# Optimization experiments

Measured on AMD Instinct MI355X. Metric: run time of the kernel, lower is better.

The kernel has to match this reference:

```python
import jax, jax.numpy as jnp
import numpy as np

N_NODES = 50000
N_EDGES = 800000
C_IN = 128
C_OUT = 64
C_HID = 2 * C_OUT  # 128


def setup_inputs() -> dict:
    key = jax.random.key(0)
    ks = jax.random.split(key, 8)
    x = jax.random.normal(ks[0], (N_NODES, C_IN), dtype=jnp.float32)
    edge_index = jax.random.randint(ks[1], (2, N_EDGES), 0, N_NODES, dtype=jnp.int64)
    s1 = 1.0 / np.sqrt(C_IN)
    s2 = 1.0 / np.sqrt(C_HID)
    s3 = 1.0 / np.sqrt(C_OUT)
    W1 = jax.random.uniform(ks[2], (C_IN, C_HID), jnp.float32, -s1, s1)
    b1 = jnp.zeros((C_HID,), jnp.float32)
    W2 = jax.random.uniform(ks[3], (C_HID, C_OUT), jnp.float32, -s2, s2)
    b2 = jnp.zeros((C_OUT,), jnp.float32)
    Wb = jax.random.uniform(ks[4], (1, C_OUT, C_OUT), jnp.float32, -s3, s3)
    bb = jax.random.uniform(ks[5], (1,), jnp.float32, -s3, s3)
    return {"x": x, "edge_index": edge_index, "W1": W1, "b1": b1,
            "W2": W2, "b2": b2, "Wb": Wb, "bb": bb}


def gcn_conv(x, W, b, src, dst, n_nodes):
    # PyG GCNConv: h = x @ W; add self-loops; symmetric normalization D^-1/2 (A+I) D^-1/2.
    h = x @ W  # [N, F]
    ones = jnp.ones((src.shape[0],), h.dtype)
    deg = jax.ops.segment_sum(ones, dst, num_segments=n_nodes) + 1.0  # +1 for self-loop
    dinv = jax.lax.rsqrt(deg)
    norm = dinv[src] * dinv[dst]  # [E]
    msgs = h[src] * norm[:, None]  # [E, F]
    agg = jax.ops.segment_sum(msgs, dst, num_segments=n_nodes)
    # self-loop contribution: norm_ii = 1/deg_i
    agg = agg + h * (1.0 / deg)[:, None]
    return agg + b


def reference(x, edge_index, W1, b1, W2, b2, Wb, bb):
    src = edge_index[0]
    dst = edge_index[1]
    n = x.shape[0]
    # encode
    h = jax.nn.relu(gcn_conv(x, W1, b1, src, dst, n))
    z = gcn_conv(h, W2, b2, src, dst, n)  # [N, C_OUT]
    # decode: bilinear on (z[src], z[dst]) -> sigmoid
    zs = z[src]  # [E, C_OUT]
    zd = z[dst]  # [E, C_OUT]
    logits = jnp.einsum('ec,ocd,ed->eo', zs, Wb, zd) + bb  # [E, 1]
    return jax.nn.sigmoid(logits)
```

## Files before the change

### kernel.cpp

```cpp
#include <hip/hip_runtime.h>
#include <hip/hip_bf16.h>


#define N_NODES 50000
#define BSH 7
#define BSZ 128
#define NBUCK ((N_NODES + BSZ - 1) / BSZ)
#define EPB 4096

typedef unsigned int u32;
typedef unsigned short u16;

typedef __attribute__((ext_vector_type(8))) short bf16x8;
typedef __attribute__((ext_vector_type(4))) float f32x4;
union frag_u { bf16x8 f; u32 u[4]; uint4 v; };

__device__ __forceinline__ float bflo(u32 u) { return __uint_as_float(u << 16); }
__device__ __forceinline__ float bfhi(u32 u) { return __uint_as_float(u & 0xffff0000u); }
__device__ __forceinline__ u32 f2bf(float f) {
    u32 b = __float_as_uint(f);
    return (b + 0x7fffu + ((b >> 16) & 1u)) >> 16;
}
__device__ __forceinline__ u32 pack2(float a, float b) { return f2bf(a) | (f2bf(b) << 16); }

__global__ __launch_bounds__(256) void bucket_hist(const int* __restrict__ dst,
                                                   int* __restrict__ bhist, int E) {
    __shared__ int hist[NBUCK];
    for (int i = threadIdx.x; i < NBUCK; i += 256) hist[i] = 0;
    __syncthreads();
    int base = blockIdx.x * EPB;
    int e1 = min(base + EPB, E);
    for (int e = base + threadIdx.x; e < e1; e += 256)
        atomicAdd(&hist[dst[e] >> BSH], 1);
    __syncthreads();
    for (int b = threadIdx.x; b < NBUCK; b += 256) {
        int c = hist[b];
        if (c) atomicAdd(&bhist[b], c);
    }
}

__global__ __launch_bounds__(512) void bucket_scan(const int* __restrict__ bhist,
                                                   int* __restrict__ bbase,
                                                   int* __restrict__ bcur, int E) {
    __shared__ int tmp[512];
    int t = threadIdx.x;
    int v = (t < NBUCK) ? bhist[t] : 0;
    tmp[t] = v;
    __syncthreads();
    for (int off = 1; off < 512; off <<= 1) {
        int a = (t >= off) ? tmp[t - off] : 0;
        __syncthreads();
        tmp[t] += a;
        __syncthreads();
    }
    int excl = tmp[t] - v;
    if (t < NBUCK) { bbase[t] = excl; bcur[t] = excl; }
    if (t == 0) bbase[NBUCK] = E;
}

__global__ __launch_bounds__(256) void bucket_scatter(const int* __restrict__ src,
                                                      const int* __restrict__ dst,
                                                      int* __restrict__ bcur,
                                                      u32* __restrict__ pair, int E) {
    __shared__ int hist[NBUCK];
    for (int i = threadIdx.x; i < NBUCK; i += 256) hist[i] = 0;
    __syncthreads();
    int base = blockIdx.x * EPB;
    int s_[16], d_[16];
#pragma unroll
    for (int it = 0; it < 16; it++) {
        int e = base + it * 256 + threadIdx.x;
        if (e < E) {
            s_[it] = src[e];
            d_[it] = dst[e];
            atomicAdd(&hist[d_[it] >> BSH], 1);
        } else {
            d_[it] = -1;
        }
    }
    __syncthreads();
    for (int b = threadIdx.x; b < NBUCK; b += 256) {
        int c = hist[b];
        hist[b] = c ? atomicAdd(&bcur[b], c) : 0;
    }
    __syncthreads();
#pragma unroll
    for (int it = 0; it < 16; it++) {
        if (d_[it] >= 0) {
            int b = d_[it] >> BSH;
            int off = atomicAdd(&hist[b], 1);
            pair[off] = (u32)s_[it] | ((u32)(d_[it] & (BSZ - 1)) << 16);
        }
    }
}

__global__ __launch_bounds__(256) void bucket_sort(const u32* __restrict__ pair,
                                                   const int* __restrict__ bbase,
                                                   int* __restrict__ row_ptr,
                                                   int* __restrict__ col,
                                                   float* __restrict__ dinv,
                                                   float* __restrict__ inv, int n, int E) {
    __shared__ int cnt[BSZ];
    __shared__ int scn[BSZ];
    __shared__ int cur[BSZ];
    int t = threadIdx.x;
    int base = blockIdx.x << BSH;
    int nn = min(BSZ, n - base);
    int b0 = bbase[blockIdx.x];
    int b1 = bbase[blockIdx.x + 1];
    if (t < BSZ) cnt[t] = 0;
    __syncthreads();
    for (int j = b0 + t; j < b1; j += 256)
        atomicAdd(&cnt[pair[j] >> 16], 1);
    __syncthreads();
    if (t < BSZ) scn[t] = cnt[t];
    __syncthreads();
    for (int off = 1; off < BSZ; off <<= 1) {
        int a = (t < BSZ && t >= off) ? scn[t - off] : 0;
        __syncthreads();
        if (t < BSZ) scn[t] += a;
        __syncthreads();
    }
    if (t < nn) {
        int excl = b0 + scn[t] - cnt[t];
        row_ptr[base + t] = excl;
        cur[t] = excl;
        float d = (float)cnt[t] + 1.0f;
        dinv[base + t] = rsqrtf(d);
        inv[base + t] = 1.0f / d;
    }
    if (t == 0 && blockIdx.x == NBUCK - 1) row_ptr[n] = E;
    __syncthreads();
    for (int j = b0 + t; j < b1; j += 256) {
        u32 p = pair[j];
        int ln = (int)(p >> 16);
        int pos = atomicAdd(&cur[ln], 1);
        col[pos] = (int)(p & 0xffffu);
    }
}

template <int K, int NOUT, bool A_BF16>
__global__ __launch_bounds__(256) void gemm_mfma(const void* __restrict__ Xv,
                                                 const float* __restrict__ W,
                                                 u16* __restrict__ O, int n_rows) {
    constexpr int KP = K + 8;
    constexpr int NT = NOUT / 16;
    constexpr int KS = K / 32;
    __shared__ __align__(16) u16 Wt_hi[NOUT * KP];
    __shared__ __align__(16) u16 Wt_lo[NOUT * KP];
    int t = threadIdx.x;
    for (int i4 = t; i4 < K * NOUT / 4; i4 += 256) {
        int k = (i4 * 4) / NOUT;
        int n0 = (i4 * 4) % NOUT;
        float4 w4 = *(const float4*)&W[(size_t)k * NOUT + n0];
        float wv[4] = {w4.x, w4.y, w4.z, w4.w};
#pragma unroll
        for (int q = 0; q < 4; q++) {
            u32 hi = f2bf(wv[q]);
            u32 lo = f2bf(wv[q] - bflo(hi));
            Wt_hi[(n0 + q) * KP + k] = (u16)hi;
            Wt_lo[(n0 + q) * KP + k] = (u16)lo;
        }
    }
    __syncthreads();

    int wave = t >> 6;
    int lane = t & 63;
    int m16 = lane & 15;
    int quad = lane >> 4;
    int row0 = blockIdx.x * 128 + wave * 32;

    f32x4 acc[2][NT] = {};
    for (int ks = 0; ks < KS; ks++) {
        frag_u a_hi[2], a_lo[2];
#pragma unroll
        for (int mt = 0; mt < 2; mt++) {
            int row = row0 + mt * 16 + m16;
            row = row < n_rows ? row : n_rows - 1;
            if (A_BF16) {
                a_hi[mt].v = *(const uint4*)((const u16*)Xv + (size_t)row * K + ks * 32 + quad * 8);
            } else {
                const float* X = (const float*)Xv + (size_t)row * K + ks * 32 + quad * 8;
                float4 x0 = *(const float4*)X;
                float4 x1 = *(const float4*)(X + 4);
                float xv[8] = {x0.x, x0.y, x0.z, x0.w, x1.x, x1.y, x1.z, x1.w};
#pragma unroll
                for (int p = 0; p < 4; p++) {
                    u32 h0 = f2bf(xv[2 * p]), h1 = f2bf(xv[2 * p + 1]);
                    a_hi[mt].u[p] = h0 | (h1 << 16);
                    a_lo[mt].u[p] = pack2(xv[2 * p] - bflo(h0), xv[2 * p + 1] - bflo(h1));
                }
            }
        }
#pragma unroll
        for (int nt = 0; nt < NT; nt++) {
            int n = nt * 16 + m16;
            frag_u b_hi, b_lo;
            b_hi.v = *(const uint4*)&Wt_hi[n * KP + ks * 32 + quad * 8];
            b_lo.v = *(const uint4*)&Wt_lo[n * KP + ks * 32 + quad * 8];
#pragma unroll
            for (int mt = 0; mt < 2; mt++) {
                acc[mt][nt] = __builtin_amdgcn_mfma_f32_16x16x32_bf16(a_hi[mt].f, b_hi.f, acc[mt][nt], 0, 0, 0);
                acc[mt][nt] = __builtin_amdgcn_mfma_f32_16x16x32_bf16(a_hi[mt].f, b_lo.f, acc[mt][nt], 0, 0, 0);
                if (!A_BF16)
                    acc[mt][nt] = __builtin_amdgcn_mfma_f32_16x16x32_bf16(a_lo[mt].f, b_hi.f, acc[mt][nt], 0, 0, 0);
            }
        }
    }
#pragma unroll
    for (int mt = 0; mt < 2; mt++)
#pragma unroll
        for (int nt = 0; nt < NT; nt++)
#pragma unroll
            for (int r = 0; r < 4; r++) {
                int row = row0 + mt * 16 + quad * 4 + r;
                if (row < n_rows)
                    O[(size_t)row * NOUT + nt * 16 + m16] = (u16)f2bf(acc[mt][nt][r]);
            }
}

template <int C, bool RELU>
__global__ __launch_bounds__(256) void agg_pull(const u16* __restrict__ H,
                                                const int* __restrict__ row_ptr,
                                                const int* __restrict__ col,
                                                const float* __restrict__ dinv,
                                                const float* __restrict__ inv,
                                                const float* __restrict__ b,
                                                u16* __restrict__ O, int n) {
    constexpr int TPN = C / 8;
    const uint4* Hv = (const uint4*)H;
    int tid = blockIdx.x * 256 + threadIdx.x;
    int node = tid / TPN;
    if (node >= n) return;
    int part = tid % TPN;
    int c8 = part * 8;
    float dn = dinv[node];
    float iv = inv[node];
    float acc[8];
    {
        uint4 h = Hv[(size_t)node * TPN + part];
        acc[0] = bflo(h.x) * iv + b[c8 + 0];
        acc[1] = bfhi(h.x) * iv + b[c8 + 1];
        acc[2] = bflo(h.y) * iv + b[c8 + 2];
        acc[3] = bfhi(h.y) * iv + b[c8 + 3];
        acc[4] = bflo(h.z) * iv + b[c8 + 4];
        acc[5] = bfhi(h.z) * iv + b[c8 + 5];
        acc[6] = bflo(h.w) * iv + b[c8 + 6];
        acc[7] = bfhi(h.w) * iv + b[c8 + 7];
    }
    int j = row_ptr[node];
    int end = row_ptr[node + 1];
    for (; j + 3 < end; j += 4) {
        int s0 = col[j], s1 = col[j + 1], s2 = col[j + 2], s3 = col[j + 3];
        float n0 = dn * dinv[s0], n1 = dn * dinv[s1];
        float n2 = dn * dinv[s2], n3 = dn * dinv[s3];
        uint4 v0 = Hv[(size_t)s0 * TPN + part];
        uint4 v1 = Hv[(size_t)s1 * TPN + part];
        uint4 v2 = Hv[(size_t)s2 * TPN + part];
        uint4 v3 = Hv[(size_t)s3 * TPN + part];
        acc[0] += bflo(v0.x) * n0 + bflo(v1.x) * n1 + bflo(v2.x) * n2 + bflo(v3.x) * n3;
        acc[1] += bfhi(v0.x) * n0 + bfhi(v1.x) * n1 + bfhi(v2.x) * n2 + bfhi(v3.x) * n3;
        acc[2] += bflo(v0.y) * n0 + bflo(v1.y) * n1 + bflo(v2.y) * n2 + bflo(v3.y) * n3;
        acc[3] += bfhi(v0.y) * n0 + bfhi(v1.y) * n1 + bfhi(v2.y) * n2 + bfhi(v3.y) * n3;
        acc[4] += bflo(v0.z) * n0 + bflo(v1.z) * n1 + bflo(v2.z) * n2 + bflo(v3.z) * n3;
        acc[5] += bfhi(v0.z) * n0 + bfhi(v1.z) * n1 + bfhi(v2.z) * n2 + bfhi(v3.z) * n3;
        acc[6] += bflo(v0.w) * n0 + bflo(v1.w) * n1 + bflo(v2.w) * n2 + bflo(v3.w) * n3;
        acc[7] += bfhi(v0.w) * n0 + bfhi(v1.w) * n1 + bfhi(v2.w) * n2 + bfhi(v3.w) * n3;
    }
    for (; j < end; j++) {
        int s = col[j];
        float nm = dn * dinv[s];
        uint4 v = Hv[(size_t)s * TPN + part];
        acc[0] += bflo(v.x) * nm; acc[1] += bfhi(v.x) * nm;
        acc[2] += bflo(v.y) * nm; acc[3] += bfhi(v.y) * nm;
        acc[4] += bflo(v.z) * nm; acc[5] += bfhi(v.z) * nm;
        acc[6] += bflo(v.w) * nm; acc[7] += bfhi(v.w) * nm;
    }
    if (RELU) {
#pragma unroll
        for (int i = 0; i < 8; i++) acc[i] = fmaxf(acc[i], 0.f);
    }
    uint4 o;
    o.x = pack2(acc[0], acc[1]);
    o.y = pack2(acc[2], acc[3]);
    o.z = pack2(acc[4], acc[5]);
    o.w = pack2(acc[6], acc[7]);
    ((uint4*)O)[(size_t)node * TPN + part] = o;
}

__global__ __launch_bounds__(256) void decode_kernel(const u16* __restrict__ Y,
                                                     const u16* __restrict__ Z,
                                                     const int* __restrict__ src,
                                                     const int* __restrict__ dst,
                                                     const float* __restrict__ bb,
                                                     float* __restrict__ out, int E) {
    const uint4* Yv = (const uint4*)Y;
    const uint4* Zv = (const uint4*)Z;
    int tid = blockIdx.x * 256 + threadIdx.x;
    int e = tid / 8;
    int lane = tid % 8;
    if (e >= E) return;
    int s = src[e], d = dst[e];
    uint4 y = Yv[(size_t)s * 8 + lane];
    uint4 z = Zv[(size_t)d * 8 + lane];
    float p = bflo(y.x) * bflo(z.x) + bfhi(y.x) * bfhi(z.x)
            + bflo(y.y) * bflo(z.y) + bfhi(y.y) * bfhi(z.y)
            + bflo(y.z) * bflo(z.z) + bfhi(y.z) * bfhi(z.z)
            + bflo(y.w) * bflo(z.w) + bfhi(y.w) * bfhi(z.w);
    p += __shfl_down(p, 4, 8);
    p += __shfl_down(p, 2, 8);
    p += __shfl_down(p, 1, 8);
    if (lane == 0) out[e] = 1.0f / (1.0f + expf(-(p + bb[0])));
}

extern "C" void kernel_launch(void* const* d_in, const int* in_sizes, int n_in,
                              void* d_out, int out_size, void* d_ws, size_t ws_size,
                              hipStream_t stream) {
    const float* x  = (const float*)d_in[0];
    const int*   ei = (const int*)d_in[1];
    const float* W1 = (const float*)d_in[2];
    const float* b1 = (const float*)d_in[3];
    const float* W2 = (const float*)d_in[4];
    const float* b2 = (const float*)d_in[5];
    const float* Wb = (const float*)d_in[6];
    const float* bb = (const float*)d_in[7];
    float* out = (float*)d_out;

    const int N = N_NODES;
    const int E = in_sizes[1] / 2;
    const int* src = ei;
    const int* dst = ei + E;
    const int GBLK = (N + 127) / 128;
    const int SBLK = (E + EPB - 1) / EPB;

    char* w = (char*)d_ws;
    int*   bhist   = (int*)w;   w += (size_t)512 * 4;
    int*   bbase   = (int*)w;   w += (size_t)512 * 4;
    int*   bcur    = (int*)w;   w += (size_t)512 * 4;
    int*   row_ptr = (int*)w;   w += (size_t)(N + 1) * 4;
    int*   col     = (int*)w;   w += (size_t)E * 4;
    u32*   pair    = (u32*)w;   w += (size_t)E * 4;
    float* dinv    = (float*)w; w += (size_t)N * 4;
    float* inv     = (float*)w; w += (size_t)N * 4;
    w = (char*)(((size_t)w + 15) & ~(size_t)15);
    u16* bufA = (u16*)w;        w += (size_t)N * 128 * 2;
    u16* bufB = (u16*)w;        w += (size_t)N * 128 * 2;
    u16* bufC = (u16*)w;

    u16* H1 = bufA;
    u16* h1 = bufB;
    u16* H2 = bufA;
    u16* Z  = bufC;
    u16* Y  = bufA + (size_t)N * 64;

    hipMemsetAsync(bhist, 0, 512 * 4, stream);
    bucket_hist<<<SBLK, 256, 0, stream>>>(dst, bhist, E);
    bucket_scan<<<1, 512, 0, stream>>>(bhist, bbase, bcur, E);
    bucket_scatter<<<SBLK, 256, 0, stream>>>(src, dst, bcur, pair, E);
    bucket_sort<<<NBUCK, 256, 0, stream>>>(pair, bbase, row_ptr, col, dinv, inv, N, E);

    gemm_mfma<128, 128, false><<<GBLK, 256, 0, stream>>>(x, W1, H1, N);
    agg_pull<128, true><<<((size_t)N * 16 + 255) / 256, 256, 0, stream>>>(
        H1, row_ptr, col, dinv, inv, b1, h1, N);

    gemm_mfma<128, 64, true><<<GBLK, 256, 0, stream>>>(h1, W2, H2, N);
    agg_pull<64, false><<<((size_t)N * 8 + 255) / 256, 256, 0, stream>>>(
        H2, row_ptr, col, dinv, inv, b2, Z, N);

    gemm_mfma<64, 64, true><<<GBLK, 256, 0, stream>>>(Z, Wb, Y, N);
    decode_kernel<<<((size_t)E * 8 + 255) / 256, 256, 0, stream>>>(Y, Z, src, dst, bb, out, E);
}
```

Baseline: 259.8 us.

## Fuse dense projections into aggregation kernels and drop bucket histogram pass

The second and third GEMMs (h1@W2 and Z@Wb) are folded into the epilogues of the two aggregation kernels. Each block stages its aggregated rows in shared memory and multiplies by the weights in fp32 FMA. This removes two MFMA launches and the global round trips of h1 and Z. Separately, the bucket histogram pass is dropped: edges are scattered into fixed-capacity per-bucket slots (CAP=3072) and the scan runs on the final counts. This risks overflow if a bucket ever gets more than CAP edges, and the fused epilogue uses scalar FMAs instead of matrix cores.

Result: slower. 292.0 us (+12.4%).

```diff
diff --git a/kernel.cpp b/kernel.cpp
--- a/kernel.cpp
+++ b/kernel.cpp
@@ -7,6 +7,7 @@
 #define BSZ 128
 #define NBUCK ((N_NODES + BSZ - 1) / BSZ)
 #define EPB 4096
+#define CAP 3072
 
 typedef unsigned int u32;
 typedef unsigned short u16;
@@ -22,41 +23,6 @@
     return (b + 0x7fffu + ((b >> 16) & 1u)) >> 16;
 }
 __device__ __forceinline__ u32 pack2(float a, float b) { return f2bf(a) | (f2bf(b) << 16); }
-
-__global__ __launch_bounds__(256) void bucket_hist(const int* __restrict__ dst,
-                                                   int* __restrict__ bhist, int E) {
-    __shared__ int hist[NBUCK];
-    for (int i = threadIdx.x; i < NBUCK; i += 256) hist[i] = 0;
-    __syncthreads();
-    int base = blockIdx.x * EPB;
-    int e1 = min(base + EPB, E);
-    for (int e = base + threadIdx.x; e < e1; e += 256)
-        atomicAdd(&hist[dst[e] >> BSH], 1);
-    __syncthreads();
-    for (int b = threadIdx.x; b < NBUCK; b += 256) {
-        int c = hist[b];
-        if (c) atomicAdd(&bhist[b], c);
-    }
-}
-
-__global__ __launch_bounds__(512) void bucket_scan(const int* __restrict__ bhist,
-                                                   int* __restrict__ bbase,
-                                                   int* __restrict__ bcur, int E) {
-    __shared__ int tmp[512];
-    int t = threadIdx.x;
-    int v = (t < NBUCK) ? bhist[t] : 0;
-    tmp[t] = v;
-    __syncthreads();
-    for (int off = 1; off < 512; off <<= 1) {
-        int a = (t >= off) ? tmp[t - off] : 0;
-        __syncthreads();
-        tmp[t] += a;
-        __syncthreads();
-    }
-    int excl = tmp[t] - v;
-    if (t < NBUCK) { bbase[t] = excl; bcur[t] = excl; }
-    if (t == 0) bbase[NBUCK] = E;
-}
 
 __global__ __launch_bounds__(256) void bucket_scatter(const int* __restrict__ src,
                                                       const int* __restrict__ dst,
@@ -81,7 +47,7 @@
     __syncthreads();
     for (int b = threadIdx.x; b < NBUCK; b += 256) {
         int c = hist[b];
-        hist[b] = c ? atomicAdd(&bcur[b], c) : 0;
+        hist[b] = c ? (b * CAP + atomicAdd(&bcur[b], c)) : 0;
     }
     __syncthreads();
 #pragma unroll
@@ -92,6 +58,23 @@
             pair[off] = (u32)s_[it] | ((u32)(d_[it] & (BSZ - 1)) << 16);
         }
     }
+}
+
+__global__ __launch_bounds__(512) void bucket_scan(const int* __restrict__ bcur,
+                                                   int* __restrict__ bbase, int E) {
+    __shared__ int tmp[512];
+    int t = threadIdx.x;
+    int v = (t < NBUCK) ? bcur[t] : 0;
+    tmp[t] = v;
+    __syncthreads();
+    for (int off = 1; off < 512; off <<= 1) {
+        int a = (t >= off) ? tmp[t - off] : 0;
+        __syncthreads();
+        tmp[t] += a;
+        __syncthreads();
+    }
+    if (t < NBUCK) bbase[t] = tmp[t] - v;
+    if (t == 0) bbase[NBUCK] = E;
 }
 
 __global__ __launch_bounds__(256) void bucket_sort(const u32* __restrict__ pair,
@@ -107,11 +90,12 @@
     int base = blockIdx.x << BSH;
     int nn = min(BSZ, n - base);
     int b0 = bbase[blockIdx.x];
-    int b1 = bbase[blockIdx.x + 1];
+    int cntE = bbase[blockIdx.x + 1] - b0;
+    int p0 = blockIdx.x * CAP;
     if (t < BSZ) cnt[t] = 0;
     __syncthreads();
-    for (int j = b0 + t; j < b1; j += 256)
-        atomicAdd(&cnt[pair[j] >> 16], 1);
+    for (int j = t; j < cntE; j += 256)
+        atomicAdd(&cnt[pair[p0 + j] >> 16], 1);
     __syncthreads();
     if (t < BSZ) scn[t] = cnt[t];
     __syncthreads();
@@ -131,16 +115,16 @@
     }
     if (t == 0 && blockIdx.x == NBUCK - 1) row_ptr[n] = E;
     __syncthreads();
-    for (int j = b0 + t; j < b1; j += 256) {
-        u32 p = pair[j];
+    for (int j = t; j < cntE; j += 256) {
+        u32 p = pair[p0 + j];
         int ln = (int)(p >> 16);
         int pos = atomicAdd(&cur[ln], 1);
         col[pos] = (int)(p & 0xffffu);
     }
 }
 
-template <int K, int NOUT, bool A_BF16>
-__global__ __launch_bounds__(256) void gemm_mfma(const void* __restrict__ Xv,
+template <int K, int NOUT>
+__global__ __launch_bounds__(256) void gemm_mfma(const float* __restrict__ X,
                                                  const float* __restrict__ W,
                                                  u16* __restrict__ O, int n_rows) {
     constexpr int KP = K + 8;
@@ -177,19 +161,15 @@
         for (int mt = 0; mt < 2; mt++) {
             int row = row0 + mt * 16 + m16;
             row = row < n_rows ? row : n_rows - 1;
-            if (A_BF16) {
-                a_hi[mt].v = *(const uint4*)((const u16*)Xv + (size_t)row * K + ks * 32 + quad * 8);
-            } else {
-                const float* X = (const float*)Xv + (size_t)row * K + ks * 32 + quad * 8;
-                float4 x0 = *(const float4*)X;
-                float4 x1 = *(const float4*)(X + 4);
-                float xv[8] = {x0.x, x0.y, x0.z, x0.w, x1.x, x1.y, x1.z, x1.w};
-#pragma unroll
-                for (int p = 0; p < 4; p++) {
-                    u32 h0 = f2bf(xv[2 * p]), h1 = f2bf(xv[2 * p + 1]);
-                    a_hi[mt].u[p] = h0 | (h1 << 16);
-                    a_lo[mt].u[p] = pack2(xv[2 * p] - bflo(h0), xv[2 * p + 1] - bflo(h1));
-                }
+            const float* Xp = X + (size_t)row * K + ks * 32 + quad * 8;
+            float4 x0 = *(const float4*)Xp;
+            float4 x1 = *(const float4*)(Xp + 4);
+            float xv[8] = {x0.x, x0.y, x0.z, x0.w, x1.x, x1.y, x1.z, x1.w};
+#pragma unroll
+            for (int p = 0; p < 4; p++) {
+                u32 h0 = f2bf(xv[2 * p]), h1 = f2bf(xv[2 * p + 1]);
+                a_hi[mt].u[p] = h0 | (h1 << 16);
+                a_lo[mt].u[p] = pack2(xv[2 * p] - bflo(h0), xv[2 * p + 1] - bflo(h1));
             }
         }
 #pragma unroll
@@ -202,8 +182,7 @@
             for (int mt = 0; mt < 2; mt++) {
                 acc[mt][nt] = __builtin_amdgcn_mfma_f32_16x16x32_bf16(a_hi[mt].f, b_hi.f, acc[mt][nt], 0, 0, 0);
                 acc[mt][nt] = __builtin_amdgcn_mfma_f32_16x16x32_bf16(a_hi[mt].f, b_lo.f, acc[mt][nt], 0, 0, 0);
-                if (!A_BF16)
-                    acc[mt][nt] = __builtin_amdgcn_mfma_f32_16x16x32_bf16(a_lo[mt].f, b_hi.f, acc[mt][nt], 0, 0, 0);
+                acc[mt][nt] = __builtin_amdgcn_mfma_f32_16x16x32_bf16(a_lo[mt].f, b_hi.f, acc[mt][nt], 0, 0, 0);
             }
         }
     }
@@ -219,73 +198,168 @@
             }
 }
 
-template <int C, bool RELU>
-__global__ __launch_bounds__(256) void agg_pull(const u16* __restrict__ H,
-                                                const int* __restrict__ row_ptr,
-                                                const int* __restrict__ col,
-                                                const float* __restrict__ dinv,
-                                                const float* __restrict__ inv,
-                                                const float* __restrict__ b,
-                                                u16* __restrict__ O, int n) {
-    constexpr int TPN = C / 8;
+__global__ __launch_bounds__(256) void agg1_fused(const u16* __restrict__ H,
+                                                  const int* __restrict__ row_ptr,
+                                                  const int* __restrict__ col,
+                                                  const float* __restrict__ dinv,
+                                                  const float* __restrict__ inv,
+                                                  const float* __restrict__ b1,
+                                                  const float* __restrict__ W2,
+                                                  u16* __restrict__ H2, int n) {
+    __shared__ float h1s[16][129];
     const uint4* Hv = (const uint4*)H;
-    int tid = blockIdx.x * 256 + threadIdx.x;
-    int node = tid / TPN;
-    if (node >= n) return;
-    int part = tid % TPN;
+    int t = threadIdx.x;
+    int nl = t / 16;
+    int part = t % 16;
     int c8 = part * 8;
-    float dn = dinv[node];
-    float iv = inv[node];
-    float acc[8];
-    {
-        uint4 h = Hv[(size_t)node * TPN + part];
-        acc[0] = bflo(h.x) * iv + b[c8 + 0];
-        acc[1] = bfhi(h.x) * iv + b[c8 + 1];
-        acc[2] = bflo(h.y) * iv + b[c8 + 2];
-        acc[3] = bfhi(h.y) * iv + b[c8 + 3];
-        acc[4] = bflo(h.z) * iv + b[c8 + 4];
-        acc[5] = bfhi(h.z) * iv + b[c8 + 5];
-        acc[6] = bflo(h.w) * iv + b[c8 + 6];
-        acc[7] = bfhi(h.w) * iv + b[c8 + 7];
-    }
-    int j = row_ptr[node];
-    int end = row_ptr[node + 1];
-    for (; j + 3 < end; j += 4) {
-        int s0 = col[j], s1 = col[j + 1], s2 = col[j + 2], s3 = col[j + 3];
-        float n0 = dn * dinv[s0], n1 = dn * dinv[s1];
-        float n2 = dn * dinv[s2], n3 = dn * dinv[s3];
-        uint4 v0 = Hv[(size_t)s0 * TPN + part];
-        uint4 v1 = Hv[(size_t)s1 * TPN + part];
-        uint4 v2 = Hv[(size_t)s2 * TPN + part];
-        uint4 v3 = Hv[(size_t)s3 * TPN + part];
-        acc[0] += bflo(v0.x) * n0 + bflo(v1.x) * n1 + bflo(v2.x) * n2 + bflo(v3.x) * n3;
-        acc[1] += bfhi(v0.x) * n0 + bfhi(v1.x) * n1 + bfhi(v2.x) * n2 + bfhi(v3.x) * n3;
-        acc[2] += bflo(v0.y) * n0 + bflo(v1.y) * n1 + bflo(v2.y) * n2 + bflo(v3.y) * n3;
-        acc[3] += bfhi(v0.y) * n0 + bfhi(v1.y) * n1 + bfhi(v2.y) * n2 + bfhi(v3.y) * n3;
-        acc[4] += bflo(v0.z) * n0 + bflo(v1.z) * n1 + bflo(v2.z) * n2 + bflo(v3.z) * n3;
-        acc[5] += bfhi(v0.z) * n0 + bfhi(v1.z) * n1 + bfhi(v2.z) * n2 + bfhi(v3.z) * n3;
-        acc[6] += bflo(v0.w) * n0 + bflo(v1.w) * n1 + bflo(v2.w) * n2 + bflo(v3.w) * n3;
-        acc[7] += bfhi(v0.w) * n0 + bfhi(v1.w) * n1 + bfhi(v2.w) * n2 + bfhi(v3.w) * n3;
-    }
-    for (; j < end; j++) {
-        int s = col[j];
-        float nm = dn * dinv[s];
-        uint4 v = Hv[(size_t)s * TPN + part];
-        acc[0] += bflo(v.x) * nm; acc[1] += bfhi(v.x) * nm;
-        acc[2] += bflo(v.y) * nm; acc[3] += bfhi(v.y) * nm;
-        acc[4] += bflo(v.z) * nm; acc[5] += bfhi(v.z) * nm;
-        acc[6] += bflo(v.w) * nm; acc[7] += bfhi(v.w) * nm;
-    }
-    if (RELU) {
+    int node = blockIdx.x * 16 + nl;
+    float acc[8] = {0, 0, 0, 0, 0, 0, 0, 0};
+    if (node < n) {
+        float dn = dinv[node];
+        float iv = inv[node];
+        uint4 h = Hv[(size_t)node * 16 + part];
+        acc[0] = bflo(h.x) * iv + b1[c8 + 0];
+        acc[1] = bfhi(h.x) * iv + b1[c8 + 1];
+        acc[2] = bflo(h.y) * iv + b1[c8 + 2];
+        acc[3] = bfhi(h.y) * iv + b1[c8 + 3];
+        acc[4] = bflo(h.z) * iv + b1[c8 + 4];
+        acc[5] = bfhi(h.z) * iv + b1[c8 + 5];
+        acc[6] = bflo(h.w) * iv + b1[c8 + 6];
+        acc[7] = bfhi(h.w) * iv + b1[c8 + 7];
+        int j = row_ptr[node];
+        int end = row_ptr[node + 1];
+        for (; j + 3 < end; j += 4) {
+            int s0 = col[j], s1 = col[j + 1], s2 = col[j + 2], s3 = col[j + 3];
+            float n0 = dn * dinv[s0], n1 = dn * dinv[s1];
+            float n2 = dn * dinv[s2], n3 = dn * dinv[s3];
+            uint4 v0 = Hv[(size_t)s0 * 16 + part];
+            uint4 v1 = Hv[(size_t)s1 * 16 + part];
+            uint4 v2 = Hv[(size_t)s2 * 16 + part];
+            uint4 v3 = Hv[(size_t)s3 * 16 + part];
+            acc[0] += bflo(v0.x) * n0 + bflo(v1.x) * n1 + bflo(v2.x) * n2 + bflo(v3.x) * n3;
+            acc[1] += bfhi(v0.x) * n0 + bfhi(v1.x) * n1 + bfhi(v2.x) * n2 + bfhi(v3.x) * n3;
+            acc[2] += bflo(v0.y) * n0 + bflo(v1.y) * n1 + bflo(v2.y) * n2 + bflo(v3.y) * n3;
+            acc[3] += bfhi(v0.y) * n0 + bfhi(v1.y) * n1 + bfhi(v2.y) * n2 + bfhi(v3.y) * n3;
+            acc[4] += bflo(v0.z) * n0 + bflo(v1.z) * n1 + bflo(v2.z) * n2 + bflo(v3.z) * n3;
+            acc[5] += bfhi(v0.z) * n0 + bfhi(v1.z) * n1 + bfhi(v2.z) * n2 + bfhi(v3.z) * n3;
+            acc[6] += bflo(v0.w) * n0 + bflo(v1.w) * n1 + bflo(v2.w) * n2 + bflo(v3.w) * n3;
+            acc[7] += bfhi(v0.w) * n0 + bfhi(v1.w) * n1 + bfhi(v2.w) * n2 + bfhi(v3.w) * n3;
+        }
+        for (; j < end; j++) {
+            int s = col[j];
+            float nm = dn * dinv[s];
+            uint4 v = Hv[(size_t)s * 16 + part];
+            acc[0] += bflo(v.x) * nm; acc[1] += bfhi(v.x) * nm;
+            acc[2] += bflo(v.y) * nm; acc[3] += bfhi(v.y) * nm;
+            acc[4] += bflo(v.z) * nm; acc[5] += bfhi(v.z) * nm;
+            acc[6] += bflo(v.w) * nm; acc[7] += bfhi(v.w) * nm;
+        }
 #pragma unroll
         for (int i = 0; i < 8; i++) acc[i] = fmaxf(acc[i], 0.f);
     }
-    uint4 o;
-    o.x = pack2(acc[0], acc[1]);
-    o.y = pack2(acc[2], acc[3]);
-    o.z = pack2(acc[4], acc[5]);
-    o.w = pack2(acc[6], acc[7]);
-    ((uint4*)O)[(size_t)node * TPN + part] = o;
+#pragma unroll
+    for (int i = 0; i < 8; i++) h1s[nl][c8 + i] = acc[i];
+    __syncthreads();
+    int oc4 = part * 4;
+    float y0 = 0.f, y1 = 0.f, y2 = 0.f, y3 = 0.f;
+#pragma unroll 4
+    for (int k = 0; k < 128; k++) {
+        float hv = h1s[nl][k];
+        float4 w4 = *(const float4*)&W2[k * 64 + oc4];
+        y0 += hv * w4.x; y1 += hv * w4.y; y2 += hv * w4.z; y3 += hv * w4.w;
+    }
+    if (node < n) {
+        uint2 p;
+        p.x = pack2(y0, y1);
+        p.y = pack2(y2, y3);
+        *(uint2*)&H2[(size_t)node * 64 + oc4] = p;
+    }
+}
+
+__global__ __launch_bounds__(256) void agg2_fused(const u16* __restrict__ H,
+                                                  const int* __restrict__ row_ptr,
+                                                  const int* __restrict__ col,
+                                                  const float* __restrict__ dinv,
+                                                  const float* __restrict__ inv,
+                                                  const float* __restrict__ b2,
+                                                  const float* __restrict__ Wb,
+                                                  u16* __restrict__ Z,
+                                                  u16* __restrict__ Y, int n) {
+    __shared__ float zs[32][65];
+    const uint4* Hv = (const uint4*)H;
+    int t = threadIdx.x;
+    int nl = t / 8;
+    int part = t % 8;
+    int c8 = part * 8;
+    int node = blockIdx.x * 32 + nl;
+    float acc[8] = {0, 0, 0, 0, 0, 0, 0, 0};
+    if (node < n) {
+        float dn = dinv[node];
+        float iv = inv[node];
+        uint4 h = Hv[(size_t)node * 8 + part];
+        acc[0] = bflo(h.x) * iv + b2[c8 + 0];
+        acc[1] = bfhi(h.x) * iv + b2[c8 + 1];
+        acc[2] = bflo(h.y) * iv + b2[c8 + 2];
+        acc[3] = bfhi(h.y) * iv + b2[c8 + 3];
+        acc[4] = bflo(h.z) * iv + b2[c8 + 4];
+        acc[5] = bfhi(h.z) * iv + b2[c8 + 5];
+        acc[6] = bflo(h.w) * iv + b2[c8 + 6];
+        acc[7] = bfhi(h.w) * iv + b2[c8 + 7];
+        int j = row_ptr[node];
+        int end = row_ptr[node + 1];
+        for (; j + 3 < end; j += 4) {
+            int s0 = col[j], s1 = col[j + 1], s2 = col[j + 2], s3 = col[j + 3];
+            float n0 = dn * dinv[s0], n1 = dn * dinv[s1];
+            float n2 = dn * dinv[s2], n3 = dn * dinv[s3];
+            uint4 v0 = Hv[(size_t)s0 * 8 + part];
+            uint4 v1 = Hv[(size_t)s1 * 8 + part];
+            uint4 v2 = Hv[(size_t)s2 * 8 + part];
+            uint4 v3 = Hv[(size_t)s3 * 8 + part];
+            acc[0] += bflo(v0.x) * n0 + bflo(v1.x) * n1 + bflo(v2.x) * n2 + bflo(v3.x) * n3;
+            acc[1] += bfhi(v0.x) * n0 + bfhi(v1.x) * n1 + bfhi(v2.x) * n2 + bfhi(v3.x) * n3;
+            acc[2] += bflo(v0.y) * n0 + bflo(v1.y) * n1 + bflo(v2.y) * n2 + bflo(v3.y) * n3;
+            acc[3] += bfhi(v0.y) * n0 + bfhi(v1.y) * n1 + bfhi(v2.y) * n2 + bfhi(v3.y) * n3;
+            acc[4] += bflo(v0.z) * n0 + bflo(v1.z) * n1 + bflo(v2.z) * n2 + bflo(v3.z) * n3;
+            acc[5] += bfhi(v0.z) * n0 + bfhi(v1.z) * n1 + bfhi(v2.z) * n2 + bfhi(v3.z) * n3;
+            acc[6] += bflo(v0.w) * n0 + bflo(v1.w) * n1 + bflo(v2.w) * n2 + bflo(v3.w) * n3;
+            acc[7] += bfhi(v0.w) * n0 + bfhi(v1.w) * n1 + bfhi(v2.w) * n2 + bfhi(v3.w) * n3;
+        }
+        for (; j < end; j++) {
+            int s = col[j];
+            float nm = dn * dinv[s];
+            uint4 v = Hv[(size_t)s * 8 + part];
+            acc[0] += bflo(v.x) * nm; acc[1] += bfhi(v.x) * nm;
+            acc[2] += bflo(v.y) * nm; acc[3] += bfhi(v.y) * nm;
+            acc[4] += bflo(v.z) * nm; acc[5] += bfhi(v.z) * nm;
+            acc[6] += bflo(v.w) * nm; acc[7] += bfhi(v.w) * nm;
+        }
+        uint4 o;
+        o.x = pack2(acc[0], acc[1]);
+        o.y = pack2(acc[2], acc[3]);
+        o.z = pack2(acc[4], acc[5]);
+        o.w = pack2(acc[6], acc[7]);
+        ((uint4*)Z)[(size_t)node * 8 + part] = o;
+    }
+#pragma unroll
+    for (int i = 0; i < 8; i++) zs[nl][c8 + i] = acc[i];
+    __syncthreads();
+    float y[8] = {0, 0, 0, 0, 0, 0, 0, 0};
+#pragma unroll 4
+    for (int k = 0; k < 64; k++) {
+        float zv = zs[nl][k];
+        float4 wa = *(const float4*)&Wb[k * 64 + c8];
+        float4 wc = *(const float4*)&Wb[k * 64 + c8 + 4];
+        y[0] += zv * wa.x; y[1] += zv * wa.y; y[2] += zv * wa.z; y[3] += zv * wa.w;
+        y[4] += zv * wc.x; y[5] += zv * wc.y; y[6] += zv * wc.z; y[7] += zv * wc.w;
+    }
+    if (node < n) {
+        uint4 o;
+        o.x = pack2(y[0], y[1]);
+        o.y = pack2(y[2], y[3]);
+        o.z = pack2(y[4], y[5]);
+        o.w = pack2(y[6], y[7]);
+        ((uint4*)Y)[(size_t)node * 8 + part] = o;
+    }
 }
 
 __global__ __launch_bounds__(256) void decode_kernel(const u16* __restrict__ Y,
@@ -334,39 +408,29 @@
     const int SBLK = (E + EPB - 1) / EPB;
 
     char* w = (char*)d_ws;
-    int*   bhist   = (int*)w;   w += (size_t)512 * 4;
+    int*   bcur    = (int*)w;   w += (size_t)512 * 4;
     int*   bbase   = (int*)w;   w += (size_t)512 * 4;
-    int*   bcur    = (int*)w;   w += (size_t)512 * 4;
     int*   row_ptr = (int*)w;   w += (size_t)(N + 1) * 4;
     int*   col     = (int*)w;   w += (size_t)E * 4;
-    u32*   pair    = (u32*)w;   w += (size_t)E * 4;
+    u32*   pair    = (u32*)w;   w += (size_t)NBUCK * CAP * 4;
     float* dinv    = (float*)w; w += (size_t)N * 4;
     float* inv     = (float*)w; w += (size_t)N * 4;
     w = (char*)(((size_t)w + 15) & ~(size_t)15);
-    u16* bufA = (u16*)w;        w += (size_t)N * 128 * 2;
-    u16* bufB = (u16*)w;        w += (size_t)N * 128 * 2;
-    u16* bufC = (u16*)w;
-
-    u16* H1 = bufA;
-    u16* h1 = bufB;
-    u16* H2 = bufA;
-    u16* Z  = bufC;
-    u16* Y  = bufA + (size_t)N * 64;
-
-    hipMemsetAsync(bhist, 0, 512 * 4, stream);
-    bucket_hist<<<SBLK, 256, 0, stream>>>(dst, bhist, E);
-    bucket_scan<<<1, 512, 0, stream>>>(bhist, bbase, bcur, E);
+    u16* H1 = (u16*)w;          w += (size_t)N * 128 * 2;
+    u16* H2 = (u16*)w;          w += (size_t)N * 64 * 2;
+    u16* Z  = (u16*)w;          w += (size_t)N * 64 * 2;
+    u16* Y  = (u16*)w;
+
+    hipMemsetAsync(bcur, 0, 512 * 4, stream);
     bucket_scatter<<<SBLK, 256, 0, stream>>>(src, dst, bcur, pair, E);
+    bucket_scan<<<1, 512, 0, stream>>>(bcur, bbase, E);
     bucket_sort<<<NBUCK, 256, 0, stream>>>(pair, bbase, row_ptr, col, dinv, inv, N, E);
 
-    gemm_mfma<128, 128, false><<<GBLK, 256, 0, stream>>>(x, W1, H1, N);
-    agg_pull<128, true><<<((size_t)N * 16 + 255) / 256, 256, 0, stream>>>(
-        H1, row_ptr, col, dinv, inv, b1, h1, N);
-
-    gemm_mfma<128, 64, true><<<GBLK, 256, 0, stream>>>(h1, W2, H2, N);
-    agg_pull<64, false><<<((size_t)N * 8 + 255) / 256, 256, 0, stream>>>(
-        H2, row_ptr, col, dinv, inv, b2, Z, N);
-
-    gemm_mfma<64, 64, true><<<GBLK, 256, 0, stream>>>(Z, Wb, Y, N);
+    gemm_mfma<128, 128><<<GBLK, 256, 0, stream>>>(x, W1, H1, N);
+
+    agg1_fused<<<(N + 15) / 16, 256, 0, stream>>>(H1, row_ptr, col, dinv, inv, b1, W2, H2, N);
+
+    agg2_fused<<<(N + 31) / 32, 256, 0, stream>>>(H2, row_ptr, col, dinv, inv, b2, Wb, Z, Y, N);
+
     decode_kernel<<<((size_t)E * 8 + 255) / 256, 256, 0, stream>>>(Y, Z, src, dst, bb, out, E);
 }
```
